# Optimization experiments

Hardware: AMD Instinct MI355X
Metric: run time of the kernel (lower is better)

The kernel has to match this reference:

```python
import jax, jax.numpy as jnp
import numpy as np

N_NODES = 100000
H_DIM = 128
N_RELS = 90   # num_rels*2 inside RGCN
N_BASES = 4
N_EDGES = 800000


def setup_inputs() -> dict:
    key = jax.random.key(0)
    k_emb, k_w, k_comp, k_r, k_norm, k_src, k_dst, k_b = jax.random.split(key, 8)
    h = jnp.arange(N_NODES, dtype=jnp.int64 if jax.config.jax_enable_x64 else jnp.int32)
    r = jax.random.randint(k_r, (N_EDGES,), 0, N_RELS)
    norm = jax.random.uniform(k_norm, (N_EDGES, 1), dtype=jnp.float32)
    src = jax.random.randint(k_src, (N_EDGES,), 0, N_NODES)
    dst = jax.random.randint(k_dst, (N_EDGES,), 0, N_NODES)
    # learned params (embedding table stands in for the word2vec-initialized table)
    emb_table = jax.random.normal(k_emb, (N_NODES, H_DIM), dtype=jnp.float32) * 0.02
    weight = jax.random.normal(k_w, (N_BASES, H_DIM, H_DIM), dtype=jnp.float32) * (1.0 / np.sqrt(H_DIM))
    w_comp = jax.random.normal(k_comp, (N_RELS, N_BASES), dtype=jnp.float32) * 0.5
    h_bias = jnp.zeros((H_DIM,), dtype=jnp.float32)
    return {"h": h, "r": r, "norm": norm, "src": src, "dst": dst,
            "emb_table": emb_table, "weight": weight, "w_comp": w_comp, "h_bias": h_bias}


def reference(h, r, norm, src, dst, emb_table, weight, w_comp, h_bias):
    # Input layer: embedding lookup on node ids  -> [N, D]
    x = emb_table[h]
    # Basis decomposition: project node feats onto each basis once  -> [N, B, D]
    # (avoids materializing per-edge [D,D] relation matrices)
    xb = jnp.einsum('ni,bio->nbo', x, weight)
    # Per-edge message: combine basis projections with relation coefficients
    coeff = w_comp[r]                       # [E, B]
    msg = jnp.einsum('ebo,eb->eo', xb[src], coeff)   # [E, D]
    msg = msg * norm                        # edge norm [E,1]
    # scatter-mean over destination nodes
    agg = jax.ops.segment_sum(msg, dst, num_segments=N_NODES)          # [N, D]
    cnt = jax.ops.segment_sum(jnp.ones((msg.shape[0],), msg.dtype), dst,
                              num_segments=N_NODES)                    # [N]
    node_repr = agg / jnp.maximum(cnt, 1.0)[:, None]
    # bias (RelGraphConv default bias=True); activation=None, self_loop=False, dropout=0
    node_repr = node_repr + h_bias
    return node_repr
```

## Files before the change

### kernel.cpp

```cpp
#include <hip/hip_runtime.h>
#include <hip/hip_bf16.h>

#define N_NODES 100000
#define H_DIM   128
#define N_RELS  90
#define N_BASES 4
#define N_EDGES 800000
#define SCAN_NB 391
#define NBLK    6250

typedef __attribute__((ext_vector_type(8))) __bf16 bf16x8;
typedef __attribute__((ext_vector_type(4))) float  floatx4;

#define WT_OFF     0
#define CNTS_OFF   131072
#define IDF_OFF    531072
#define OFFS_OFF   531076
#define CURS_OFF   931076
#define BSUM_OFF   1331076
#define RECS_OFF   1332640

__device__ __forceinline__ float bs2f(unsigned short s) {
    union { unsigned u; float f; } x; x.u = ((unsigned)s) << 16; return x.f;
}
__device__ __forceinline__ unsigned short f2bs(float f) {
    unsigned u = __float_as_uint(f);
    return (unsigned short)((u + 0x7fffu + ((u >> 16) & 1u)) >> 16);
}
template <int ISBF>
__device__ __forceinline__ float ldT(const void* p, size_t i) {
    if (ISBF) return bs2f(((const unsigned short*)p)[i]);
    return ((const float*)p)[i];
}

template <int ISBF>
__global__ __launch_bounds__(256) void prep_count_k(const void* __restrict__ weight,
                                                    unsigned short* __restrict__ wt,
                                                    const int* __restrict__ dst,
                                                    int* __restrict__ counts,
                                                    const int* __restrict__ h,
                                                    int* __restrict__ idflag) {
    int b = blockIdx.x;
    if (b < 256) {
        int tid = b * 256 + threadIdx.x;
        int o = tid >> 9, c = tid & 511;
        int bb = c >> 7, i = c & 127;
        wt[tid] = f2bs(ldT<ISBF>(weight, (size_t)bb * 16384 + (size_t)i * 128 + o));
    } else {
        int e = (b - 256) * 256 + threadIdx.x;
        if (e < N_EDGES) atomicAdd(&counts[dst[e]], 1);
        if (e < N_NODES && h[e] != e) atomicOr(idflag, 1);
    }
}

__global__ __launch_bounds__(256) void scanA(const int* __restrict__ counts,
                                             int* __restrict__ offs, int* __restrict__ bsum) {
    __shared__ int s[256];
    int t = threadIdx.x, i = blockIdx.x * 256 + t;
    int v = (i < N_NODES) ? counts[i] : 0;
    s[t] = v; __syncthreads();
    for (int off = 1; off < 256; off <<= 1) {
        int x = (t >= off) ? s[t - off] : 0;
        __syncthreads(); s[t] += x; __syncthreads();
    }
    if (i < N_NODES) offs[i] = s[t] - v;
    if (t == 255) bsum[blockIdx.x] = s[255];
}

__global__ __launch_bounds__(256) void scanC2(int* __restrict__ offs,
                                              const int* __restrict__ bsum,
                                              int* __restrict__ cursor) {
    int b = blockIdx.x, t = threadIdx.x;
    int v = 0;
    if (t < b) v = bsum[t];
    if (t + 256 < b) v += bsum[t + 256];
    v += __shfl_down(v, 32); v += __shfl_down(v, 16);
    v += __shfl_down(v, 8);  v += __shfl_down(v, 4);
    v += __shfl_down(v, 2);  v += __shfl_down(v, 1);
    __shared__ int wsum[4];
    __shared__ int sprefix;
    if ((t & 63) == 0) wsum[t >> 6] = v;
    __syncthreads();
    if (t == 0) sprefix = wsum[0] + wsum[1] + wsum[2] + wsum[3];
    __syncthreads();
    int i = b * 256 + t;
    if (i < N_NODES) {
        int o = offs[i] + sprefix;
        offs[i] = o; cursor[i] = o;
    }
}

template <int ISBF>
__global__ __launch_bounds__(256) void fill_k(const int* __restrict__ r, const void* __restrict__ norm,
                                              const int* __restrict__ src, const int* __restrict__ dst,
                                              const int* __restrict__ h, const int* __restrict__ idflag,
                                              int* __restrict__ cursor,
                                              unsigned long long* __restrict__ recs) {
    int e = blockIdx.x * 256 + threadIdx.x;
    if (e >= N_EDGES) return;
    float nm = ldT<ISBF>(norm, e);
    int s = src[e];
    int hs = (*idflag) ? h[s] : s;
    unsigned lo = (unsigned)hs | ((unsigned)r[e] << 20);
    unsigned long long rc = (unsigned long long)lo
                          | ((unsigned long long)__float_as_uint(nm) << 32);
    int pos = atomicAdd(&cursor[dst[e]], 1);
    __builtin_nontemporal_store(rc, &recs[pos]);
}

template <int ISBF>
__global__ __launch_bounds__(256) void fused_k(const int* __restrict__ counts,
                                               const int* __restrict__ offs,
                                               const unsigned long long* __restrict__ recs,
                                               const void* __restrict__ emb,
                                               const unsigned short* __restrict__ wt,
                                               const void* __restrict__ bias,
                                               const void* __restrict__ wcomp,
                                               void* __restrict__ out) {
    __shared__ float wc[N_RELS * 4];
    __shared__ __align__(16) unsigned short y[16][520];
    for (int t = threadIdx.x; t < N_RELS * 4; t += 256) wc[t] = ldT<ISBF>(wcomp, t);
    __syncthreads();

    int t = threadIdx.x;
    int lane = t & 63;
    int w = t >> 6;
    int g = lane >> 4, j = lane & 15;
    int blk = blockIdx.x;
    int dloc = w * 4 + g;
    int d = blk * 16 + dloc;
    int deg = counts[d], start = offs[d];
    float inv = 1.0f / (float)(deg > 1 ? deg : 1);

    float acc[4][8];
#pragma unroll
    for (int b = 0; b < 4; ++b)
#pragma unroll
        for (int c = 0; c < 8; ++c) acc[b][c] = 0.f;

    int kmax = __shfl(deg, 0);
    kmax = max(kmax, __shfl(deg, 16));
    kmax = max(kmax, __shfl(deg, 32));
    kmax = max(kmax, __shfl(deg, 48));

    unsigned long long rcur[4], rnext[4];
    bf16x8  rows[4];
    floatx4 rowsf[4][2];

#pragma unroll
    for (int u = 0; u < 4; ++u)
        rcur[u] = __builtin_nontemporal_load(&recs[(u < deg) ? start + u : 0]);
    if (ISBF) {
#pragma unroll
        for (int u = 0; u < 4; ++u) {
            unsigned hx = (unsigned)rcur[u] & 0xFFFFFu;
            rows[u] = *(const bf16x8*)((const unsigned short*)emb + (size_t)hx * 128 + j * 8);
        }
    } else {
#pragma unroll
        for (int u = 0; u < 4; ++u) {
            unsigned hx = (unsigned)rcur[u] & 0xFFFFFu;
            const floatx4* f = (const floatx4*)((const float*)emb + (size_t)hx * 128 + j * 8);
            rowsf[u][0] = f[0]; rowsf[u][1] = f[1];
        }
    }
#pragma unroll
    for (int u = 0; u < 4; ++u) {
        int kk = 4 + u;
        rnext[u] = __builtin_nontemporal_load(&recs[(kk < deg) ? start + kk : 0]);
    }

    for (int k = 0; k < kmax; k += 4) {
#pragma unroll
        for (int u = 0; u < 4; ++u) {
            float x[8];
            if (ISBF) {
                bf16x8 rv = rows[u];
#pragma unroll
                for (int c = 0; c < 8; ++c) x[c] = (float)rv[c];
            } else {
                floatx4 a = rowsf[u][0], bvec = rowsf[u][1];
#pragma unroll
                for (int c = 0; c < 4; ++c) { x[c] = a[c]; x[c + 4] = bvec[c]; }
            }
            {
                unsigned hx = (unsigned)rnext[u] & 0xFFFFFu;
                if (ISBF) {
                    rows[u] = *(const bf16x8*)((const unsigned short*)emb
                                               + (size_t)hx * 128 + j * 8);
                } else {
                    const floatx4* f = (const floatx4*)((const float*)emb
                                               + (size_t)hx * 128 + j * 8);
                    rowsf[u][0] = f[0]; rowsf[u][1] = f[1];
                }
            }
            bool vld = (k + u) < deg;
            unsigned rel = ((unsigned)rcur[u] >> 20) & 0xFFFu;
            float nm = vld ? __uint_as_float((unsigned)(rcur[u] >> 32)) : 0.f;
            const float* cw = &wc[rel * 4];
            float c0 = cw[0] * nm, c1 = cw[1] * nm, c2 = cw[2] * nm, c3 = cw[3] * nm;
#pragma unroll
            for (int c = 0; c < 8; ++c) {
                acc[0][c] += c0 * x[c];
                acc[1][c] += c1 * x[c];
                acc[2][c] += c2 * x[c];
                acc[3][c] += c3 * x[c];
            }
        }
#pragma unroll
        for (int u = 0; u < 4; ++u) rcur[u] = rnext[u];
#pragma unroll
        for (int u = 0; u < 4; ++u) {
            int kk = k + 8 + u;
            rnext[u] = __builtin_nontemporal_load(&recs[(kk < deg) ? start + kk : 0]);
        }
    }

#pragma unroll
    for (int b = 0; b < 4; ++b) {
        union { unsigned short u[8]; uint4 v; } pk;
#pragma unroll
        for (int c = 0; c < 8; ++c) pk.u[c] = f2bs(acc[b][c] * inv);
        *(uint4*)&y[dloc][b * 128 + j * 8] = pk.v;
    }
    __syncthreads();

    int m = lane & 15;
    int q = lane >> 4;
    for (int half = 0; half < 2; ++half) {
        int ct = w * 2 + half;
        floatx4 accm = {0.f, 0.f, 0.f, 0.f};
        const unsigned short* bp = wt + (size_t)(ct * 16 + m) * 512 + q * 8;
#pragma unroll
        for (int kc = 0; kc < 16; ++kc) {
            bf16x8 af = *(const bf16x8*)&y[m][kc * 32 + q * 8];
            bf16x8 bf = *(const bf16x8*)(bp + kc * 32);
            accm = __builtin_amdgcn_mfma_f32_16x16x32_bf16(af, bf, accm, 0, 0, 0);
        }
#pragma unroll
        for (int v = 0; v < 4; ++v) {
            int o = ct * 16 + m;
            float val = accm[v] + ldT<ISBF>(bias, o);
            size_t oi = (size_t)(blk * 16 + q * 4 + v) * H_DIM + o;
            if (ISBF) ((unsigned short*)out)[oi] = f2bs(val);
            else      ((float*)out)[oi] = val;
        }
    }
}

template <int ISBF>
static void launch_all(const int* h, const int* r, const void* norm, const int* src,
                       const int* dst, const void* emb, const void* weight,
                       const void* wcomp, const void* bias, char* ws, void* d_out,
                       hipStream_t stream) {
    unsigned short*     wt     = (unsigned short*)(ws + WT_OFF);
    int*                counts = (int*)(ws + CNTS_OFF);
    int*                idflag = (int*)(ws + IDF_OFF);
    int*                offs   = (int*)(ws + OFFS_OFF);
    int*                cursor = (int*)(ws + CURS_OFF);
    int*                bsum   = (int*)(ws + BSUM_OFF);
    unsigned long long* recs   = (unsigned long long*)(ws + RECS_OFF);

    hipMemsetAsync(counts, 0, N_NODES * sizeof(int) + sizeof(int), stream);

    prep_count_k<ISBF><<<256 + (N_EDGES + 255) / 256, 256, 0, stream>>>(weight, wt, dst,
                                                                        counts, h, idflag);
    scanA<<<SCAN_NB, 256, 0, stream>>>(counts, offs, bsum);
    scanC2<<<SCAN_NB, 256, 0, stream>>>(offs, bsum, cursor);
    fill_k<ISBF><<<(N_EDGES + 255) / 256, 256, 0, stream>>>(r, norm, src, dst, h, idflag,
                                                            cursor, recs);
    fused_k<ISBF><<<NBLK, 256, 0, stream>>>(counts, offs, recs, emb, wt, bias, wcomp, d_out);
}

extern "C" void kernel_launch(void* const* d_in, const int* in_sizes, int n_in,
                              void* d_out, int out_size, void* d_ws, size_t ws_size,
                              hipStream_t stream) {
    const int*  h      = (const int*)d_in[0];
    const int*  r      = (const int*)d_in[1];
    const void* norm   = d_in[2];
    const int*  src    = (const int*)d_in[3];
    const int*  dst    = (const int*)d_in[4];
    const void* emb    = d_in[5];
    const void* weight = d_in[6];
    const void* wcomp  = d_in[7];
    const void* bias   = d_in[8];
    char* ws = (char*)d_ws;

    int isbf = (in_sizes[2] == (int)(N_EDGES * sizeof(unsigned short))) ? 1 : 0;

    if (isbf) launch_all<1>(h, r, norm, src, dst, emb, weight, wcomp, bias, ws, d_out, stream);
    else      launch_all<0>(h, r, norm, src, dst, emb, weight, wcomp, bias, ws, d_out, stream);
}
```

Baseline: 353.1 us.

## Make fused gather-GEMM kernel persistent with grid-stride over node tiles

```diff
diff --git a/kernel.cpp b/kernel.cpp
--- a/kernel.cpp
+++ b/kernel.cpp
@@ -8,6 +8,7 @@
 #define N_EDGES 800000
 #define SCAN_NB 391
 #define NBLK    6250
+#define FUSED_NB 2048
 
 typedef __attribute__((ext_vector_type(8))) __bf16 bf16x8;
 typedef __attribute__((ext_vector_type(4))) float  floatx4;
@@ -120,130 +121,117 @@
     __shared__ float wc[N_RELS * 4];
     __shared__ __align__(16) unsigned short y[16][520];
     for (int t = threadIdx.x; t < N_RELS * 4; t += 256) wc[t] = ldT<ISBF>(wcomp, t);
-    __syncthreads();
 
     int t = threadIdx.x;
     int lane = t & 63;
     int w = t >> 6;
     int g = lane >> 4, j = lane & 15;
-    int blk = blockIdx.x;
     int dloc = w * 4 + g;
-    int d = blk * 16 + dloc;
-    int deg = counts[d], start = offs[d];
-    float inv = 1.0f / (float)(deg > 1 ? deg : 1);
-
-    float acc[4][8];
-#pragma unroll
-    for (int b = 0; b < 4; ++b)
-#pragma unroll
-        for (int c = 0; c < 8; ++c) acc[b][c] = 0.f;
-
-    int kmax = __shfl(deg, 0);
-    kmax = max(kmax, __shfl(deg, 16));
-    kmax = max(kmax, __shfl(deg, 32));
-    kmax = max(kmax, __shfl(deg, 48));
-
-    unsigned long long rcur[4], rnext[4];
-    bf16x8  rows[4];
-    floatx4 rowsf[4][2];
-
-#pragma unroll
-    for (int u = 0; u < 4; ++u)
-        rcur[u] = __builtin_nontemporal_load(&recs[(u < deg) ? start + u : 0]);
-    if (ISBF) {
-#pragma unroll
-        for (int u = 0; u < 4; ++u) {
-            unsigned hx = (unsigned)rcur[u] & 0xFFFFFu;
-            rows[u] = *(const bf16x8*)((const unsigned short*)emb + (size_t)hx * 128 + j * 8);
-        }
-    } else {
-#pragma unroll
-        for (int u = 0; u < 4; ++u) {
-            unsigned hx = (unsigned)rcur[u] & 0xFFFFFu;
-            const floatx4* f = (const floatx4*)((const float*)emb + (size_t)hx * 128 + j * 8);
-            rowsf[u][0] = f[0]; rowsf[u][1] = f[1];
-        }
-    }
-#pragma unroll
-    for (int u = 0; u < 4; ++u) {
-        int kk = 4 + u;
-        rnext[u] = __builtin_nontemporal_load(&recs[(kk < deg) ? start + kk : 0]);
-    }
-
-    for (int k = 0; k < kmax; k += 4) {
-#pragma unroll
-        for (int u = 0; u < 4; ++u) {
-            float x[8];
-            if (ISBF) {
-                bf16x8 rv = rows[u];
-#pragma unroll
-                for (int c = 0; c < 8; ++c) x[c] = (float)rv[c];
-            } else {
-                floatx4 a = rowsf[u][0], bvec = rowsf[u][1];
-#pragma unroll
-                for (int c = 0; c < 4; ++c) { x[c] = a[c]; x[c + 4] = bvec[c]; }
-            }
-            {
-                unsigned hx = (unsigned)rnext[u] & 0xFFFFFu;
-                if (ISBF) {
-                    rows[u] = *(const bf16x8*)((const unsigned short*)emb
-                                               + (size_t)hx * 128 + j * 8);
-                } else {
-                    const floatx4* f = (const floatx4*)((const float*)emb
-                                               + (size_t)hx * 128 + j * 8);
-                    rowsf[u][0] = f[0]; rowsf[u][1] = f[1];
-                }
-            }
-            bool vld = (k + u) < deg;
-            unsigned rel = ((unsigned)rcur[u] >> 20) & 0xFFFu;
-            float nm = vld ? __uint_as_float((unsigned)(rcur[u] >> 32)) : 0.f;
-            const float* cw = &wc[rel * 4];
-            float c0 = cw[0] * nm, c1 = cw[1] * nm, c2 = cw[2] * nm, c3 = cw[3] * nm;
-#pragma unroll
-            for (int c = 0; c < 8; ++c) {
-                acc[0][c] += c0 * x[c];
-                acc[1][c] += c1 * x[c];
-                acc[2][c] += c2 * x[c];
-                acc[3][c] += c3 * x[c];
-            }
-        }
-#pragma unroll
-        for (int u = 0; u < 4; ++u) rcur[u] = rnext[u];
-#pragma unroll
-        for (int u = 0; u < 4; ++u) {
-            int kk = k + 8 + u;
-            rnext[u] = __builtin_nontemporal_load(&recs[(kk < deg) ? start + kk : 0]);
-        }
-    }
-
-#pragma unroll
-    for (int b = 0; b < 4; ++b) {
-        union { unsigned short u[8]; uint4 v; } pk;
-#pragma unroll
-        for (int c = 0; c < 8; ++c) pk.u[c] = f2bs(acc[b][c] * inv);
-        *(uint4*)&y[dloc][b * 128 + j * 8] = pk.v;
-    }
-    __syncthreads();
-
     int m = lane & 15;
     int q = lane >> 4;
-    for (int half = 0; half < 2; ++half) {
-        int ct = w * 2 + half;
-        floatx4 accm = {0.f, 0.f, 0.f, 0.f};
-        const unsigned short* bp = wt + (size_t)(ct * 16 + m) * 512 + q * 8;
-#pragma unroll
-        for (int kc = 0; kc < 16; ++kc) {
-            bf16x8 af = *(const bf16x8*)&y[m][kc * 32 + q * 8];
-            bf16x8 bf = *(const bf16x8*)(bp + kc * 32);
-            accm = __builtin_amdgcn_mfma_f32_16x16x32_bf16(af, bf, accm, 0, 0, 0);
+
+    for (int blk = blockIdx.x; blk < NBLK; blk += FUSED_NB) {
+        int d = blk * 16 + dloc;
+        int deg = counts[d], start = offs[d];
+        float inv = 1.0f / (float)(deg > 1 ? deg : 1);
+
+        float acc[4][8];
+#pragma unroll
+        for (int b = 0; b < 4; ++b)
+#pragma unroll
+            for (int c = 0; c < 8; ++c) acc[b][c] = 0.f;
+
+        int kmax = __shfl(deg, 0);
+        kmax = max(kmax, __shfl(deg, 16));
+        kmax = max(kmax, __shfl(deg, 32));
+        kmax = max(kmax, __shfl(deg, 48));
+
+        unsigned long long rcur[4];
+#pragma unroll
+        for (int u = 0; u < 4; ++u)
+            rcur[u] = __builtin_nontemporal_load(&recs[(u < deg) ? start + u : 0]);
+
+        for (int k = 0; k < kmax; k += 4) {
+            unsigned long long rnext[4];
+#pragma unroll
+            for (int u = 0; u < 4; ++u) {
+                int kk = k + 4 + u;
+                rnext[u] = __builtin_nontemporal_load(&recs[(kk < deg) ? start + kk : 0]);
+            }
+            bf16x8  rb[4];
+            floatx4 rf[4][2];
+            if (ISBF) {
+#pragma unroll
+                for (int u = 0; u < 4; ++u) {
+                    unsigned hx = (unsigned)rcur[u] & 0xFFFFFu;
+                    rb[u] = *(const bf16x8*)((const unsigned short*)emb
+                                             + (size_t)hx * 128 + j * 8);
+                }
+            } else {
+#pragma unroll
+                for (int u = 0; u < 4; ++u) {
+                    unsigned hx = (unsigned)rcur[u] & 0xFFFFFu;
+                    const floatx4* f = (const floatx4*)((const float*)emb
+                                             + (size_t)hx * 128 + j * 8);
+                    rf[u][0] = f[0]; rf[u][1] = f[1];
+                }
+            }
+#pragma unroll
+            for (int u = 0; u < 4; ++u) {
+                bool v = (k + u) < deg;
+                unsigned rel = ((unsigned)rcur[u] >> 20) & 0xFFFu;
+                float nm = v ? __uint_as_float((unsigned)(rcur[u] >> 32)) : 0.f;
+                const float* cw = &wc[rel * 4];
+                float c0 = cw[0] * nm, c1 = cw[1] * nm, c2 = cw[2] * nm, c3 = cw[3] * nm;
+                float x[8];
+                if (ISBF) {
+#pragma unroll
+                    for (int c = 0; c < 8; ++c) x[c] = (float)rb[u][c];
+                } else {
+#pragma unroll
+                    for (int c = 0; c < 4; ++c) { x[c] = rf[u][0][c]; x[c + 4] = rf[u][1][c]; }
+                }
+#pragma unroll
+                for (int c = 0; c < 8; ++c) {
+                    acc[0][c] += c0 * x[c];
+                    acc[1][c] += c1 * x[c];
+                    acc[2][c] += c2 * x[c];
+                    acc[3][c] += c3 * x[c];
+                }
+            }
+#pragma unroll
+            for (int u = 0; u < 4; ++u) rcur[u] = rnext[u];
         }
-#pragma unroll
-        for (int v = 0; v < 4; ++v) {
-            int o = ct * 16 + m;
-            float val = accm[v] + ldT<ISBF>(bias, o);
-            size_t oi = (size_t)(blk * 16 + q * 4 + v) * H_DIM + o;
-            if (ISBF) ((unsigned short*)out)[oi] = f2bs(val);
-            else      ((float*)out)[oi] = val;
+
+        __syncthreads();
+
+#pragma unroll
+        for (int b = 0; b < 4; ++b) {
+            union { unsigned short u[8]; uint4 v; } pk;
+#pragma unroll
+            for (int c = 0; c < 8; ++c) pk.u[c] = f2bs(acc[b][c] * inv);
+            *(uint4*)&y[dloc][b * 128 + j * 8] = pk.v;
+        }
+        __syncthreads();
+
+        for (int half = 0; half < 2; ++half) {
+            int ct = w * 2 + half;
+            floatx4 accm = {0.f, 0.f, 0.f, 0.f};
+            const unsigned short* bp = wt + (size_t)(ct * 16 + m) * 512 + q * 8;
+#pragma unroll
+            for (int kc = 0; kc < 16; ++kc) {
+                bf16x8 af = *(const bf16x8*)&y[m][kc * 32 + q * 8];
+                bf16x8 bf = *(const bf16x8*)(bp + kc * 32);
+                accm = __builtin_amdgcn_mfma_f32_16x16x32_bf16(af, bf, accm, 0, 0, 0);
+            }
+#pragma unroll
+            for (int v = 0; v < 4; ++v) {
+                int o = ct * 16 + m;
+                float val = accm[v] + ldT<ISBF>(bias, o);
+                size_t oi = (size_t)(blk * 16 + q * 4 + v) * H_DIM + o;
+                if (ISBF) ((unsigned short*)out)[oi] = f2bs(val);
+                else      ((float*)out)[oi] = val;
+            }
         }
     }
 }
@@ -269,7 +257,7 @@
     scanC2<<<SCAN_NB, 256, 0, stream>>>(offs, bsum, cursor);
     fill_k<ISBF><<<(N_EDGES + 255) / 256, 256, 0, stream>>>(r, norm, src, dst, h, idflag,
                                                             cursor, recs);
-    fused_k<ISBF><<<NBLK, 256, 0, stream>>>(counts, offs, recs, emb, wt, bias, wcomp, d_out);
+    fused_k<ISBF><<<FUSED_NB, 256, 0, stream>>>(counts, offs, recs, emb, wt, bias, wcomp, d_out);
 }
 
 extern "C" void kernel_launch(void* const* d_in, const int* in_sizes, int n_in,
```

Result: no change. 348.4 us (-1.3%).
